# Kernel optimization log

Measured on AMD Instinct MI355X. Metric: run time of the kernel, lower is better.

## Reference

```python
import jax, jax.numpy as jnp
import numpy as np

# SLAY feature-map hyperparams (must match init_kwargs)
H, D, P, M, R = 4, 128, 16, 32, 2   # heads, head_dim, poly_dim, num_features, quad nodes
EPS = 1e-6
C = 2.0 + EPS
_nodes, _weights = np.polynomial.laguerre.laggauss(R)
QUAD_NODES = jnp.asarray(_nodes, jnp.float32) / C
QUAD_WEIGHTS = jnp.asarray(_weights, jnp.float32) / C

VOCAB, NUM_LABELS, EMBED_DIM = 100000, 32768, 512
B, S, K = 512, 64, 5


def slay_features(x, omega, anchors):
    """SLAY feature map: tensor product of anchored polynomial and PRF features.
    x: [N, EMBED_DIM] -> [N, R*H*P*M]"""
    N = x.shape[0]
    xr = x.reshape(N, H, D)
    xn = xr / jnp.clip(jnp.linalg.norm(xr, axis=-1, keepdims=True), 1e-6)  # safe_normalize
    # anchored polynomial features: [N, H, P]
    poly_feat = jnp.einsum('nhd,pd->nhp', xn, anchors) ** 2 / jnp.sqrt(float(P))
    # positive random features with Gauss-Laguerre quadrature: [R, N, H, M]
    prf_proj = jnp.einsum('nhd,rhdm->rnhm', xn, omega)
    s = QUAD_NODES.reshape(R, 1, 1, 1)
    sqrt_2s = jnp.sqrt(2.0 * jnp.clip(s, 0))
    prf_feat = jnp.exp(jnp.clip(prf_proj * sqrt_2s - s, -10.0, 10.0)) / jnp.sqrt(float(M))
    prf_feat = prf_feat * jnp.sqrt(jnp.clip(QUAD_WEIGHTS.reshape(R, 1, 1, 1), 0))
    # tensor-product fusion: [N, R, H, P, M] -> [N, R*H*P*M]
    fused = jnp.einsum('nhp,rnhm->nrhpm', poly_feat, prf_feat)
    return fused.reshape(N, -1)


def mean_embedding(indices, mask, embedding_table):
    embeds = embedding_table[indices]                       # [B, S, E]
    sum_embeds = jnp.sum(embeds * mask[:, :, None], axis=1)  # [B, E]
    sum_mask = jnp.sum(mask, axis=1, keepdims=True)
    return sum_embeds / jnp.clip(sum_mask, 1e-9)


def setup_inputs() -> dict:
    key = jax.random.key(0)
    k1, k2, k3, k4, k5, k6 = jax.random.split(key, 6)
    indices = jax.random.randint(k1, (B, S), 0, VOCAB)
    mask = jnp.ones((B, S), dtype=jnp.float32)
    labels = jax.random.randint(k2, (B, K), 0, NUM_LABELS)
    label_mask = jnp.ones((B, K), dtype=jnp.float32)
    embedding_table = jax.random.normal(k3, (VOCAB, EMBED_DIM), dtype=jnp.float32) * 0.02
    classifier_kernel = jax.random.normal(k4, (EMBED_DIM, NUM_LABELS), dtype=jnp.float32) * 0.02
    omega = jax.random.normal(k5, (R, H, D, M), dtype=jnp.float32)
    anchors = jax.random.normal(k6, (P, D), dtype=jnp.float32)
    anchors = anchors / jnp.linalg.norm(anchors, axis=-1, keepdims=True)
    return {"indices": indices, "mask": mask, "labels": labels, "label_mask": label_mask,
            "embedding_table": embedding_table, "classifier_kernel": classifier_kernel,
            "omega": omega, "anchors": anchors}


def reference(indices, mask, labels, label_mask, embedding_table, classifier_kernel, omega, anchors):
    query = mean_embedding(indices, mask, embedding_table)            # [B, E]
    phi_query = slay_features(query, omega, anchors)                  # [B, F]
    W_vecs = classifier_kernel.T                                      # [L, E]
    phi_W = slay_features(W_vecs, omega, anchors)                     # [L, F]  (dominant cost)
    Z_approx_vec = jnp.sum(phi_W, axis=0)                             # [F]
    denom = jnp.dot(phi_query, Z_approx_vec) + 1e-6                   # [B]
    log_Z = jnp.log(denom)
    safe_labels = jnp.maximum(labels, 0)
    W_pos = W_vecs[safe_labels]                                       # [B, K, E]
    phi_w_pos = slay_features(W_pos.reshape(-1, EMBED_DIM), omega, anchors).reshape(B, K, -1)
    nums = jnp.sum(phi_w_pos * phi_query[:, None, :], axis=-1) + 1e-6  # [B, K]
    log_probs = jnp.log(nums) - log_Z[:, None]
    loss_total = -jnp.sum(log_probs * label_mask)
    return loss_total / B
```

## Files before the change

kernel.cpp:

```cpp
#include <hip/hip_runtime.h>
#include <math.h>


namespace {
constexpr double Cq  = 2.0 + 1e-6;
constexpr double QN0 = 0.5857864376269049  / Cq;
constexpr double QN1 = 3.414213562373095   / Cq;
constexpr double QW0 = 0.8535533905932738  / Cq;
constexpr double QW1 = 0.14644660940672624 / Cq;

constexpr size_t OFF_POLYQ = 0;
constexpr size_t OFF_PRFQ  = 32768;
constexpr size_t OFF_Z     = OFF_PRFQ + 131072;
constexpr size_t OFF_ANCT  = OFF_Z + 4096;
constexpr size_t OFF_WPACK = OFF_ANCT + 2048;
constexpr size_t OFF_FEAT  = OFF_WPACK + 49152;
}

__global__ void k_setup(const float* __restrict__ anchors,
                        const float* __restrict__ omega,
                        float* __restrict__ Z, float* __restrict__ out,
                        float* __restrict__ anct, float* __restrict__ Wpack)
{
    int t = blockIdx.x * 256 + threadIdx.x;
    if (t < 4096) Z[t] = 0.f;
    if (t == 0) out[0] = 0.f;
    if (t < 2048) {
        int p = t & 15, d = t >> 4;
        anct[t] = anchors[p * 128 + d];
    }
    for (int i = t; i < 4 * 4 * 128 * 24; i += 16384) {
        int iw = i % 24;
        int hwd = i / 24;
        int d = hwd & 127;
        int hw = hwd >> 7;
        int w = hw & 3, h = hw >> 2;
        int o = w * 21 + iw;
        float v = 0.f;
        if (iw < 21 && o < 80) {
            if (o < 16) v = anchors[o * 128 + d];
            else {
                int r = (o - 16) >> 5, m = (o - 16) & 31;
                v = omega[(((r * 4 + h) * 128) + d) * 32 + m];
            }
        }
        Wpack[i] = v;
    }
}

__global__ void __launch_bounds__(256, 4)
k_ab(const int* __restrict__ idx, const float* __restrict__ mask,
     const float* __restrict__ emb, const float* __restrict__ ck,
     const float* __restrict__ omega, const float* __restrict__ anct,
     const float* __restrict__ Wpack,
     float* __restrict__ polyq, float* __restrict__ prfq,
     float* __restrict__ Z, float* __restrict__ feat)
{
    __shared__ float smem[8192];
    __shared__ float rnS[4];

    int t = threadIdx.x;
    int lane = t & 63;
    int w = t >> 6;
    int bid = blockIdx.x;

    const float s_[2] = {(float)QN0, (float)QN1};
    const float g_[2] = {sqrtf(2.0f * (float)QN0), sqrtf(2.0f * (float)QN1)};
    const float c_[2] = {sqrtf((float)QW0) * 0.17677669529663687f,
                         sqrtf((float)QW1) * 0.17677669529663687f};

    if (bid < 512) {
        int b = bid;
        float2 acc = make_float2(0.f, 0.f);
        float msum = 0.f;
#pragma unroll 8
        for (int s = 0; s < 64; ++s) {
            float mv = mask[b * 64 + s];
            const float2* row = (const float2*)(emb + (size_t)idx[b * 64 + s] * 512);
            float2 v = row[t];
            acc.x = fmaf(mv, v.x, acc.x);
            acc.y = fmaf(mv, v.y, acc.y);
            msum += mv;
        }
        float inv = 1.0f / fmaxf(msum, 1e-9f);
        smem[2 * t]     = acc.x * inv;
        smem[2 * t + 1] = acc.y * inv;
        __syncthreads();
        {
            float v0 = smem[w * 128 + lane], v1 = smem[w * 128 + 64 + lane];
            float ss = fmaf(v0, v0, v1 * v1);
#pragma unroll
            for (int o = 1; o < 64; o <<= 1) ss += __shfl_xor(ss, o, 64);
            if (lane == 0) rnS[w] = 1.0f / fmaxf(sqrtf(ss), 1e-6f);
        }
        __syncthreads();
        for (int tau = t; tau < 320; tau += 256) {
            int h = tau / 80, j = tau - h * 80;
            const float* xh = smem + h * 128;
            if (j < 16) {
                float a = 0.f;
                for (int d = 0; d < 128; ++d) a = fmaf(xh[d], anct[d * 16 + j], a);
                float v = a * rnS[h];
                polyq[(b * 4 + h) * 16 + j] = v * v * 0.25f;
            } else {
                int rj = j - 16, r = rj >> 5, m = rj & 31;
                const float* om = omega + ((size_t)(r * 4 + h) * 128) * 32 + m;
                float a = 0.f;
                for (int d = 0; d < 128; ++d) a = fmaf(xh[d], om[d * 32], a);
                float z = a * rnS[h] * g_[r] - s_[r];
                z = fminf(fmaxf(z, -10.f), 10.f);
                prfq[((b * 2 + r) * 4 + h) * 32 + m] = expf(z) * c_[r];
            }
        }
        return;
    }

    int tile = bid - 512;
    int g = tile >> 2, h = tile & 3;
    int l0 = g << 6;

    {
        const float* src = ck + (size_t)h * 128 * 32768 + l0;
#pragma unroll
        for (int k2 = 0; k2 < 32; ++k2) {
            int ix = k2 * 256 + t;
            int d = ix >> 6, lab = ix & 63;
            smem[ix] = src[(size_t)d * 32768 + lab];
        }
    }
    __syncthreads();

    int wu = __builtin_amdgcn_readfirstlane(w);
    const float* wv = Wpack + ((size_t)((h << 2) | wu) * 128) * 24;
    float acc[21] = {};
    float sumsq = 0.f;
    for (int d = 0; d < 128; ++d) {
        float xv = smem[d * 64 + lane];
        sumsq = fmaf(xv, xv, sumsq);
        const float* c = wv + d * 24;
        float4 c0 = *(const float4*)(c);
        float4 c1 = *(const float4*)(c + 4);
        float4 c2 = *(const float4*)(c + 8);
        float4 c3 = *(const float4*)(c + 12);
        float4 c4 = *(const float4*)(c + 16);
        float cl = c[20];
        acc[0]  = fmaf(xv, c0.x, acc[0]);  acc[1]  = fmaf(xv, c0.y, acc[1]);
        acc[2]  = fmaf(xv, c0.z, acc[2]);  acc[3]  = fmaf(xv, c0.w, acc[3]);
        acc[4]  = fmaf(xv, c1.x, acc[4]);  acc[5]  = fmaf(xv, c1.y, acc[5]);
        acc[6]  = fmaf(xv, c1.z, acc[6]);  acc[7]  = fmaf(xv, c1.w, acc[7]);
        acc[8]  = fmaf(xv, c2.x, acc[8]);  acc[9]  = fmaf(xv, c2.y, acc[9]);
        acc[10] = fmaf(xv, c2.z, acc[10]); acc[11] = fmaf(xv, c2.w, acc[11]);
        acc[12] = fmaf(xv, c3.x, acc[12]); acc[13] = fmaf(xv, c3.y, acc[13]);
        acc[14] = fmaf(xv, c3.z, acc[14]); acc[15] = fmaf(xv, c3.w, acc[15]);
        acc[16] = fmaf(xv, c4.x, acc[16]); acc[17] = fmaf(xv, c4.y, acc[17]);
        acc[18] = fmaf(xv, c4.z, acc[18]); acc[19] = fmaf(xv, c4.w, acc[19]);
        acc[20] = fmaf(xv, cl,   acc[20]);
    }
    __syncthreads();

    int o0 = wu * 21;
#pragma unroll
    for (int i = 0; i < 21; ++i) {
        int o = o0 + i;
        if (o < 80) smem[lane * 85 + o] = acc[i];
    }
    if (wu == 3) smem[lane * 85 + 80] = sumsq;
    __syncthreads();

    {
        int l = t & 63, part = t >> 6, of = part * 20;
        float rn = 1.0f / fmaxf(sqrtf(smem[l * 85 + 80]), 1e-6f);
#pragma unroll
        for (int i = 0; i < 20; ++i) {
            int o = of + i;
            float v = smem[l * 85 + o];
            if (o < 16) {
                v = v * rn;
                v = v * v * 0.25f;
            } else {
                int r = (o - 16) >> 5;
                float z = v * rn * g_[r] - s_[r];
                z = fminf(fmaxf(z, -10.f), 10.f);
                v = expf(z) * c_[r];
            }
            smem[l * 85 + o] = v;
        }
    }
    __syncthreads();

    for (int e = t; e < 5120; e += 256) {
        int j = e / 80, o = e - j * 80;
        feat[((size_t)(l0 + j) * 4 + h) * 80 + o] = smem[j * 85 + o];
    }

    if (t < 128) {
        int r = t >> 6, p0 = ((t >> 3) & 7) * 2, m0 = (t & 7) * 4;
        float z0[4] = {}, z1[4] = {};
        for (int j = 0; j < 64; ++j) {
            const float* row = smem + j * 85;
            float pa = row[p0], pb = row[p0 + 1];
            const float* pf = row + 16 + r * 32 + m0;
#pragma unroll
            for (int k2 = 0; k2 < 4; ++k2) {
                float fv = pf[k2];
                z0[k2] = fmaf(pa, fv, z0[k2]);
                z1[k2] = fmaf(pb, fv, z1[k2]);
            }
        }
        float* zb = Z + ((size_t)(r * 4 + h) * 16) * 32;
#pragma unroll
        for (int k2 = 0; k2 < 4; ++k2) {
            atomicAdd(&zb[p0 * 32 + m0 + k2],       z0[k2]);
            atomicAdd(&zb[(p0 + 1) * 32 + m0 + k2], z1[k2]);
        }
    }
}

__global__ void k_final(const float* __restrict__ polyq, const float* __restrict__ prfq,
                        const float* __restrict__ Z, const int* __restrict__ labels,
                        const float* __restrict__ lmask,
                        const float* __restrict__ feat, float* __restrict__ out)
{
    int t = threadIdx.x, lane = t & 63;
    int b = blockIdx.x * 4 + (t >> 6);

    float acc = 0.f;
    for (int i = 0; i < 64; ++i) {
        int f = i * 64 + lane;
        int m = f & 31, p = (f >> 5) & 15, hh = (f >> 9) & 3, r = f >> 11;
        float phi = polyq[(b * 4 + hh) * 16 + p] * prfq[((b * 2 + r) * 4 + hh) * 32 + m];
        acc = fmaf(phi, Z[f], acc);
    }
#pragma unroll
    for (int o = 1; o < 64; o <<= 1) acc += __shfl_xor(acc, o, 64);
    float logZb = logf(acc + 1e-6f);

    if (lane < 20) {
        int k = lane >> 2, h = lane & 3;
        int l = max(labels[b * 5 + k], 0);
        const float4* f4 = (const float4*)(feat + ((size_t)l * 4 + h) * 80);
        const float* pq = polyq + (b * 4 + h) * 16;
        const float* q0 = prfq + ((b * 2 + 0) * 4 + h) * 32;
        const float* q1 = prfq + ((b * 2 + 1) * 4 + h) * 32;

        float pd = 0.f;
#pragma unroll
        for (int j = 0; j < 4; ++j) {
            float4 fp = f4[j];
            pd = fmaf(fp.x, pq[4*j+0], pd);
            pd = fmaf(fp.y, pq[4*j+1], pd);
            pd = fmaf(fp.z, pq[4*j+2], pd);
            pd = fmaf(fp.w, pq[4*j+3], pd);
        }
        float f0 = 0.f, f1 = 0.f;
#pragma unroll
        for (int j = 0; j < 8; ++j) {
            float4 fv = f4[4 + j];
            f0 = fmaf(fv.x, q0[4*j+0], f0);
            f0 = fmaf(fv.y, q0[4*j+1], f0);
            f0 = fmaf(fv.z, q0[4*j+2], f0);
            f0 = fmaf(fv.w, q0[4*j+3], f0);
            float4 fw = f4[12 + j];
            f1 = fmaf(fw.x, q1[4*j+0], f1);
            f1 = fmaf(fw.y, q1[4*j+1], f1);
            f1 = fmaf(fw.z, q1[4*j+2], f1);
            f1 = fmaf(fw.w, q1[4*j+3], f1);
        }
        float c = pd * (f0 + f1);
        c += __shfl_xor(c, 1, 64);
        c += __shfl_xor(c, 2, 64);
        if (h == 0) {
            float val = (logf(c + 1e-6f) - logZb) * lmask[b * 5 + k];
            atomicAdd(out, val * (-1.0f / 512.0f));
        }
    }
}

extern "C" void kernel_launch(void* const* d_in, const int* in_sizes, int n_in,
                              void* d_out, int out_size, void* d_ws, size_t ws_size,
                              hipStream_t stream)
{
    const int*   indices = (const int*)  d_in[0];
    const float* mask    = (const float*)d_in[1];
    const int*   labels  = (const int*)  d_in[2];
    const float* lmask   = (const float*)d_in[3];
    const float* emb     = (const float*)d_in[4];
    const float* ck      = (const float*)d_in[5];
    const float* omega   = (const float*)d_in[6];
    const float* anchors = (const float*)d_in[7];
    float* ws  = (float*)d_ws;
    float* out = (float*)d_out;

    float* polyq = ws + OFF_POLYQ;
    float* prfq  = ws + OFF_PRFQ;
    float* Zp    = ws + OFF_Z;
    float* anct  = ws + OFF_ANCT;
    float* Wpack = ws + OFF_WPACK;
    float* feat  = ws + OFF_FEAT;

    k_setup<<<64, 256, 0, stream>>>(anchors, omega, Zp, out, anct, Wpack);
    k_ab<<<2560, 256, 0, stream>>>(indices, mask, emb, ck, omega, anct, Wpack,
                                   polyq, prfq, Zp, feat);
    k_final<<<128, 256, 0, stream>>>(polyq, prfq, Zp, labels, lmask, feat, out);
}
```

Measured before the change: 398.1 us.

## Stage packed weights in LDS, stream W rows from global, replace Z atomics with partials

The label-tile path now copies the per-head packed anchor/omega coefficients into a larger shared buffer and reads the classifier columns directly from global memory per lane, instead of staging classifier data in LDS and reading coefficients from global. The Z accumulation moves from per-tile atomicAdds to per-tile partial writes, followed by a new reduction kernel that does far fewer atomics. Occupancy bound drops from 4 to 3 blocks per CU to fit the larger shared buffer. This adds an extra kernel launch and 8 MB of partial traffic in exchange for less atomic contention and cheaper coefficient access.

```diff
diff --git a/kernel.cpp b/kernel.cpp
--- a/kernel.cpp
+++ b/kernel.cpp
@@ -14,7 +14,8 @@
 constexpr size_t OFF_Z     = OFF_PRFQ + 131072;
 constexpr size_t OFF_ANCT  = OFF_Z + 4096;
 constexpr size_t OFF_WPACK = OFF_ANCT + 2048;
-constexpr size_t OFF_FEAT  = OFF_WPACK + 49152;
+constexpr size_t OFF_ZPART = OFF_WPACK + 49152;
+constexpr size_t OFF_FEAT  = OFF_ZPART + 2097152;
 }
 
 __global__ void k_setup(const float* __restrict__ anchors,
@@ -48,16 +49,15 @@
     }
 }
 
-__global__ void __launch_bounds__(256, 4)
+__global__ void __launch_bounds__(256, 3)
 k_ab(const int* __restrict__ idx, const float* __restrict__ mask,
      const float* __restrict__ emb, const float* __restrict__ ck,
      const float* __restrict__ omega, const float* __restrict__ anct,
      const float* __restrict__ Wpack,
      float* __restrict__ polyq, float* __restrict__ prfq,
-     float* __restrict__ Z, float* __restrict__ feat)
-{
-    __shared__ float smem[8192];
-    __shared__ float rnS[4];
+     float* __restrict__ Zpart, float* __restrict__ feat)
+{
+    __shared__ float smem[12288];
 
     int t = threadIdx.x;
     int lane = t & 63;
@@ -70,6 +70,7 @@
                          sqrtf((float)QW1) * 0.17677669529663687f};
 
     if (bid < 512) {
+        float* rnS = smem + 12284;
         int b = bid;
         float2 acc = make_float2(0.f, 0.f);
         float msum = 0.f;
@@ -120,24 +121,23 @@
     int l0 = g << 6;
 
     {
-        const float* src = ck + (size_t)h * 128 * 32768 + l0;
-#pragma unroll
-        for (int k2 = 0; k2 < 32; ++k2) {
-            int ix = k2 * 256 + t;
-            int d = ix >> 6, lab = ix & 63;
-            smem[ix] = src[(size_t)d * 32768 + lab];
-        }
+        const float4* src = (const float4*)(Wpack + (size_t)h * 12288);
+        float4* dst = (float4*)smem;
+#pragma unroll
+        for (int i = 0; i < 12; ++i) dst[i * 256 + t] = src[i * 256 + t];
     }
     __syncthreads();
 
     int wu = __builtin_amdgcn_readfirstlane(w);
-    const float* wv = Wpack + ((size_t)((h << 2) | wu) * 128) * 24;
+    const float* cw = smem + wu * 3072;
+    const float* xg = ck + ((size_t)h * 128) * 32768 + l0 + lane;
     float acc[21] = {};
     float sumsq = 0.f;
+#pragma unroll 8
     for (int d = 0; d < 128; ++d) {
-        float xv = smem[d * 64 + lane];
+        float xv = xg[(size_t)d * 32768];
         sumsq = fmaf(xv, xv, sumsq);
-        const float* c = wv + d * 24;
+        const float* c = cw + d * 24;
         float4 c0 = *(const float4*)(c);
         float4 c1 = *(const float4*)(c + 4);
         float4 c2 = *(const float4*)(c + 8);
@@ -207,13 +207,25 @@
                 z1[k2] = fmaf(pb, fv, z1[k2]);
             }
         }
-        float* zb = Z + ((size_t)(r * 4 + h) * 16) * 32;
+        float* zp = Zpart + (size_t)tile * 1024;
 #pragma unroll
         for (int k2 = 0; k2 < 4; ++k2) {
-            atomicAdd(&zb[p0 * 32 + m0 + k2],       z0[k2]);
-            atomicAdd(&zb[(p0 + 1) * 32 + m0 + k2], z1[k2]);
-        }
-    }
+            zp[(r * 16 + p0) * 32 + m0 + k2]     = z0[k2];
+            zp[(r * 16 + p0 + 1) * 32 + m0 + k2] = z1[k2];
+        }
+    }
+}
+
+__global__ void k_zreduce(const float* __restrict__ Zpart, float* __restrict__ Z)
+{
+    int tid = blockIdx.x * 256 + threadIdx.x;
+    int e = tid & 1023, h = (tid >> 10) & 3, chunk = tid >> 12;
+    float sum = 0.f;
+    int g0 = chunk * 64;
+#pragma unroll 4
+    for (int g = g0; g < g0 + 64; ++g)
+        sum += Zpart[(size_t)((g << 2) | h) * 1024 + e];
+    atomicAdd(&Z[(e >> 9) * 2048 + h * 512 + (e & 511)], sum);
 }
 
 __global__ void k_final(const float* __restrict__ polyq, const float* __restrict__ prfq,
@@ -296,10 +308,12 @@
     float* Zp    = ws + OFF_Z;
     float* anct  = ws + OFF_ANCT;
     float* Wpack = ws + OFF_WPACK;
+    float* Zpart = ws + OFF_ZPART;
     float* feat  = ws + OFF_FEAT;
 
     k_setup<<<64, 256, 0, stream>>>(anchors, omega, Zp, out, anct, Wpack);
     k_ab<<<2560, 256, 0, stream>>>(indices, mask, emb, ck, omega, anct, Wpack,
-                                   polyq, prfq, Zp, feat);
+                                   polyq, prfq, Zpart, feat);
+    k_zreduce<<<128, 256, 0, stream>>>(Zpart, Zp);
     k_final<<<128, 256, 0, stream>>>(polyq, prfq, Zp, labels, lmask, feat, out);
 }
```

Result: slower. 489.7 us (+23.0%).
